# Optimization experiments

Measured on AMD Instinct MI355X. Metric: run time of the kernel, lower is better.

Reference implementation:

```python
import jax, jax.numpy as jnp
import numpy as np

N_NODES = 20000
N_EDGES = 160000
D = 1000          # out_channels of GatedGraphConv / Linear in-dim
NUM_LAYERS = 3


def setup_inputs() -> dict:
    key = jax.random.key(0)
    ks = jax.random.split(key, 10)
    x = jax.random.normal(ks[0], (N_NODES, D), dtype=jnp.float32)
    edge_index = jax.random.randint(ks[1], (2, N_EDGES), 0, N_NODES, dtype=jnp.int32)
    edge_weight = jax.random.uniform(ks[2], (N_EDGES,), dtype=jnp.float32)
    s = 1.0 / np.sqrt(D)
    weight = jax.random.uniform(ks[3], (NUM_LAYERS, D, D), minval=-s, maxval=s, dtype=jnp.float32)
    w_ih = jax.random.uniform(ks[4], (3 * D, D), minval=-s, maxval=s, dtype=jnp.float32)
    w_hh = jax.random.uniform(ks[5], (3 * D, D), minval=-s, maxval=s, dtype=jnp.float32)
    b_ih = jax.random.uniform(ks[6], (3 * D,), minval=-s, maxval=s, dtype=jnp.float32)
    b_hh = jax.random.uniform(ks[7], (3 * D,), minval=-s, maxval=s, dtype=jnp.float32)
    fc_w = jax.random.uniform(ks[8], (1, D), minval=-s, maxval=s, dtype=jnp.float32)
    fc_b = jax.random.uniform(ks[9], (1,), minval=-s, maxval=s, dtype=jnp.float32)
    return {
        "x": x, "edge_index": edge_index, "edge_weight": edge_weight,
        "weight": weight, "w_ih": w_ih, "w_hh": w_hh, "b_ih": b_ih, "b_hh": b_hh,
        "fc_w": fc_w, "fc_b": fc_b, "prob": 0,
    }


def _gru_cell(m, h, w_ih, w_hh, b_ih, b_hh):
    # torch.nn.GRUCell: gate order r, z, n
    gi = m @ w_ih.T + b_ih   # [N, 3D]
    gh = h @ w_hh.T + b_hh   # [N, 3D]
    i_r, i_z, i_n = jnp.split(gi, 3, axis=-1)
    h_r, h_z, h_n = jnp.split(gh, 3, axis=-1)
    r = jax.nn.sigmoid(i_r + h_r)
    z = jax.nn.sigmoid(i_z + h_z)
    n = jnp.tanh(i_n + r * h_n)
    return (1.0 - z) * n + z * h


def reference(x, edge_index, edge_weight, weight, w_ih, w_hh, b_ih, b_hh, fc_w, fc_b, prob):
    src = edge_index[0]
    dst = edge_index[1]
    h = x
    for layer in range(NUM_LAYERS):
        m = h @ weight[layer]                                  # [N, D]
        msg = m[src] * edge_weight[:, None]                    # [E, D]
        agg = jax.ops.segment_sum(msg, dst, num_segments=N_NODES)  # scatter-add
        h = _gru_cell(agg, h, w_ih, w_hh, b_ih, b_hh)
    h = jax.nn.relu(h)
    # F.dropout with p=prob=0 is identity (scale 1/(1-0)=1)
    return h @ fc_w.T + fc_b                                   # [N, 1]
```

## Files before the change

kernel.cpp:

```cpp
#include <hip/hip_runtime.h>

typedef unsigned short u16;
typedef unsigned int u32;
typedef unsigned long long u64;
typedef __attribute__((ext_vector_type(8))) short bf16x8;
typedef __attribute__((ext_vector_type(4))) float f32x4;

#define N_NODES 20000
#define N_EDGES 160000
#define DDIM    1000
#define KP      1024
#define SP      41200000
#define WCAT_L  6291456

__device__ __forceinline__ float b2f(u16 u) {
    union { u32 i; float f; } v; v.i = ((u32)u) << 16; return v.f;
}
__device__ __forceinline__ u16 f2b(float f) {
    union { float f; u32 i; } v; v.f = f;
    u32 r = v.i + 0x7FFFu + ((v.i >> 16) & 1u);
    return (u16)(r >> 16);
}
__device__ __forceinline__ u32 pack2(float a, float b) {
    return (u32)f2b(a) | ((u32)f2b(b) << 16);
}
__device__ __forceinline__ f32x4 mfma16(bf16x8 a, bf16x8 b, f32x4 c) {
    return __builtin_amdgcn_mfma_f32_16x16x32_bf16(a, b, c, 0, 0, 0);
}
__device__ __forceinline__ float fexp_(float x) {
    return __builtin_amdgcn_exp2f(x * 1.4426950408889634f);
}
__device__ __forceinline__ float fsigmoid_(float x) {
    return __builtin_amdgcn_rcpf(1.0f + fexp_(-x));
}
__device__ __forceinline__ float ftanh_(float x) {
    float ax = fabsf(x);
    float e = fexp_(-2.0f * ax);
    float t = (1.0f - e) * __builtin_amdgcn_rcpf(1.0f + e);
    return x >= 0.0f ? t : -t;
}

__device__ __forceinline__ void gl2lds16(const u16* g, u16* l) {
    __builtin_amdgcn_global_load_lds(
        (const __attribute__((address_space(1))) u32*)g,
        (__attribute__((address_space(3))) u32*)l, 16, 0, 0);
}
__device__ __forceinline__ u32 lds_addr(const u16* p) {
    return (u32)(uintptr_t)(const __attribute__((address_space(3))) u16*)p;
}

__global__ __launch_bounds__(256) void cvt_rows(const float* __restrict__ in,
                                                u16* __restrict__ out) {
    int r = blockIdx.x, c = threadIdx.x * 4;
    u32 o[2] = {0, 0};
    if (c < DDIM) {
        float4 v = *(const float4*)(in + (size_t)r * DDIM + c);
        o[0] = pack2(v.x, v.y); o[1] = pack2(v.z, v.w);
    }
    *(uint2*)(out + (size_t)r * KP + c) = *(const uint2*)o;
}

__global__ __launch_bounds__(256) void cvt_weights(const float* __restrict__ wih,
                                                   const float* __restrict__ W,
                                                   const float* __restrict__ whh,
                                                   u16* __restrict__ wihb,
                                                   u16* __restrict__ Wb3,
                                                   u16* __restrict__ wcat) {
    int b = blockIdx.x, c = threadIdx.x * 4;
    const float* src;
    u16* dst;
    if (b < 3000) {
        src = wih + (size_t)b * DDIM;
        dst = wihb + (size_t)b * KP;
    } else if (b < 6000) {
        int r = b - 3000;
        int l = r / 1000, row = r - l * 1000;
        src = W + (size_t)r * DDIM;
        dst = Wb3 + (size_t)l * 1048576 + (size_t)row * KP;
    } else {
        int r = b - 6000;
        int l = r / 3000, gr = r - l * 3000;
        int g = gr / 1000, n2 = gr - g * 1000;
        src = whh + (size_t)gr * DDIM;
        dst = wcat + (size_t)l * WCAT_L + ((size_t)g * 1024 + n2) * 2048 + 1024;
    }
    u32 o[2] = {0, 0};
    if (c < DDIM) {
        float4 v = *(const float4*)(src + c);
        o[0] = pack2(v.x, v.y); o[1] = pack2(v.z, v.w);
    }
    *(uint2*)(dst + c) = *(const uint2*)o;
}

__global__ __launch_bounds__(256) void count_edges(const int* __restrict__ ei,
                                                   int* __restrict__ cnt) {
    int e = blockIdx.x * 256 + threadIdx.x;
    if (e < N_EDGES) atomicAdd(&cnt[ei[N_EDGES + e]], 1);
}

__global__ __launch_bounds__(1024) void scan_offsets(const int* __restrict__ cnt,
                                                     int* __restrict__ ofs) {
    __shared__ int s[1024];
    const int CH = 20;
    int t = threadIdx.x;
    int base = t * CH;
    int loc[CH];
    int sum = 0;
    for (int j = 0; j < CH; j++) {
        int i = base + j;
        loc[j] = sum;
        sum += (i < N_NODES) ? cnt[i] : 0;
    }
    s[t] = sum;
    __syncthreads();
    for (int d = 1; d < 1024; d <<= 1) {
        int v = (t >= d) ? s[t - d] : 0;
        __syncthreads();
        s[t] += v;
        __syncthreads();
    }
    int excl = s[t] - sum;
    for (int j = 0; j < CH; j++) {
        int i = base + j;
        if (i < N_NODES) ofs[i] = excl + loc[j];
    }
    if (t == 0) ofs[N_NODES] = N_EDGES;
}

__global__ __launch_bounds__(256) void fill_buckets(const int* __restrict__ ei,
                                                    const int* __restrict__ ofs,
                                                    int* __restrict__ cur,
                                                    int* __restrict__ bkt) {
    int e = blockIdx.x * 256 + threadIdx.x;
    if (e >= N_EDGES) return;
    int d = ei[N_EDGES + e];
    int pos = atomicAdd(&cur[d], 1);
    bkt[ofs[d] + pos] = e;
}

__global__ __launch_bounds__(256) void node_agg(const int* __restrict__ ei,
                                                const float* __restrict__ ew,
                                                const int* __restrict__ ofs,
                                                const int* __restrict__ bkt,
                                                const u16* __restrict__ hsrc,
                                                u16* __restrict__ agg) {
    __shared__ int   s_src[2][32];
    __shared__ float s_w[2][32];
    __shared__ int   s_it[2];
    int tid = threadIdx.x;
    int half = tid >> 7, t = tid & 127;
    int node = blockIdx.x * 2 + half;
    int beg = ofs[node], end = ofs[node + 1];
    if (t == 0) s_it[half] = (end - beg + 31) >> 5;
    __syncthreads();
    int iters = max(s_it[0], s_it[1]);
    float acc[8] = {};
    for (int it = 0; it < iters; it++) {
        int cb = beg + it * 32;
        int n = min(32, end - cb);
        if (t < n) {
            int e = bkt[cb + t];
            s_src[half][t] = ei[e];
            s_w[half][t]   = ew[e];
        }
        __syncthreads();
        if (t < 125) {
            for (int j = 0; j < n; j++) {
                int src = s_src[half][j];
                float w = s_w[half][j];
                uint4 v = *(const uint4*)(hsrc + (size_t)src * KP + t * 8);
                const u16* p = (const u16*)&v;
#pragma unroll
                for (int k = 0; k < 8; k++) acc[k] += b2f(p[k]) * w;
            }
        }
        __syncthreads();
    }
    if (t < 125) {
        u32 o[4] = {pack2(acc[0], acc[1]), pack2(acc[2], acc[3]),
                    pack2(acc[4], acc[5]), pack2(acc[6], acc[7])};
        *(uint4*)(agg + (size_t)node * KP + t * 8) = *(const uint4*)o;
    } else if (t < 128) {
        uint4 z = {0, 0, 0, 0};
        *(uint4*)(agg + (size_t)node * KP + 1000 + (t - 125) * 8) = z;
    }
}

__global__ __launch_bounds__(256) void gemm_wc(const u16* __restrict__ A,
                                               const u16* __restrict__ Bt3,
                                               u16* __restrict__ wcat) {
    __shared__ u16 S[16384];
    int tid = threadIdx.x;
    int lane = tid & 63, wave = tid >> 6;
    int wr = wave >> 1, wc = wave & 1;
    int bid = blockIdx.x;
    int l = blockIdx.y;
    int m0 = (bid >> 3) * 128, n0 = (bid & 7) * 128;
    const u16* Bt = Bt3 + (size_t)l * 1048576;

    int aoff[4], boff[4];
#pragma unroll
    for (int i = 0; i < 4; i++) {
        int c = tid + 256 * i;
        int row = c >> 3, sl = c & 7;
        int kc = sl ^ (row & 7);
        aoff[i] = (m0 + row) * KP + kc * 8;
        boff[i] = (n0 + row) * KP + kc * 8;
    }
    f32x4 acc[4][4] = {};
    int fr = lane & 15, q = lane >> 4, sw = fr & 7;

    for (int k0 = 0; k0 < KP; k0 += 64) {
#pragma unroll
        for (int i = 0; i < 4; i++) {
            gl2lds16(A + aoff[i] + k0, &S[tid * 8 + 2048 * i]);
            gl2lds16(Bt + boff[i] + k0, &S[8192 + tid * 8 + 2048 * i]);
        }
        __syncthreads();
#pragma unroll
        for (int ks = 0; ks < 2; ks++) {
            int kx = ((ks * 4 + q) ^ sw) * 8;
            bf16x8 af[4], bf[4];
#pragma unroll
            for (int i = 0; i < 4; i++)
                af[i] = *(const bf16x8*)&S[(wr * 64 + i * 16 + fr) * 64 + kx];
#pragma unroll
            for (int j = 0; j < 4; j++)
                bf[j] = *(const bf16x8*)&S[8192 + (wc * 64 + j * 16 + fr) * 64 + kx];
#pragma unroll
            for (int i = 0; i < 4; i++)
#pragma unroll
                for (int j = 0; j < 4; j++)
                    acc[i][j] = mfma16(af[i], bf[j], acc[i][j]);
        }
        __syncthreads();
    }

    u16* wl = wcat + (size_t)l * WCAT_L;
    int cc = lane & 15, r4 = q * 4;
#pragma unroll
    for (int i = 0; i < 4; i++)
#pragma unroll
        for (int j = 0; j < 4; j++) {
            int gn = n0 + wc * 64 + j * 16 + cc;
            if (gn >= DDIM) continue;
#pragma unroll
            for (int r = 0; r < 4; r++) {
                int gm = m0 + wr * 64 + i * 16 + r4 + r;
                if (gm >= 3000) continue;
                int slab = (gm >= 2000) ? 2 : (gm >= 1000 ? 1 : 0);
                int row = gm - slab * 1000;
                wl[(size_t)slab * 2097152 + (size_t)row * 2048 + gn] =
                    f2b(acc[i][j][r]);
            }
        }
}

#define DSR(D, A)   asm volatile("ds_read_b128 %0, %1" : "=v"(D) : "v"(A))
#define DSR8(D, A)  asm volatile("ds_read_b128 %0, %1 offset:8192" : "=v"(D) : "v"(A))
#define DSR16(D, A) asm volatile("ds_read_b128 %0, %1 offset:16384" : "=v"(D) : "v"(A))
#define LGKM(N) do { asm volatile("s_waitcnt lgkmcnt(" #N ")" ::: "memory");  \
                     __builtin_amdgcn_sched_barrier(0); } while (0)
#define MF4(ACC, I, G) do {                                                   \
        ACC[I][0] = mfma16(af[I][0], wf[G][0][0], ACC[I][0]);                 \
        ACC[I][0] = mfma16(af[I][1], wf[G][0][1], ACC[I][0]);                 \
        ACC[I][1] = mfma16(af[I][0], wf[G][1][0], ACC[I][1]);                 \
        ACC[I][1] = mfma16(af[I][1], wf[G][1][1], ACC[I][1]);                 \
    } while (0)

__global__ __launch_bounds__(512, 2) void gru_fused(const u16* __restrict__ agg,
                                                    const u16* __restrict__ h,
                                                    const u16* __restrict__ wcat,
                                                    const float* __restrict__ bih,
                                                    const float* __restrict__ bhh,
                                                    u16* __restrict__ hout) {
    extern __shared__ u16 S[];
    int tid = threadIdx.x;
    int lane = tid & 63, wave = tid >> 6;
    int wr = wave >> 1, wc = wave & 1;

    int bid = blockIdx.x;
    int xcd = bid & 7;
    int s = bid >> 3;
    int panel = s >> 1, hi = s & 1;
    int m0 = panel * 256;
    int n0 = (xcd * 2 + hi) * 64;

    int aoff[4];
#pragma unroll
    for (int i = 0; i < 4; i++) {
        int c = tid + 512 * i;
        int row = c >> 3, sl = c & 7;
        int kc = sl ^ (row & 7);
        aoff[i] = (m0 + row) * KP + kc * 8;
    }
    int wrow = tid >> 3;
    int woff = (n0 + wrow) * 2048 + ((tid & 7) ^ (wrow & 7)) * 8;

    f32x4 aR[4][2] = {}, aZ[4][2] = {}, aN[4][2] = {}, aH[4][2] = {};
    int fr = lane & 15, q = lane >> 4, sw = fr & 7;
    int kx0 = (q ^ sw) * 8, kx1 = ((4 + q) ^ sw) * 8;

    u32 afa[4][2], wfa[2][2];
#pragma unroll
    for (int i = 0; i < 4; i++) {
        int ar = (wr * 64 + i * 16 + fr) * 64;
        afa[i][0] = lds_addr(&S[ar + kx0]);
        afa[i][1] = lds_addr(&S[ar + kx1]);
    }
#pragma unroll
    for (int j = 0; j < 2; j++) {
        int wcl = (wc * 32 + j * 16 + fr) * 64;
        wfa[j][0] = lds_addr(&S[32768 + wcl + kx0]);
        wfa[j][1] = lds_addr(&S[32768 + wcl + kx1]);
    }

#define STAGE(ts) do {                                                        \
        const u16* ap_ = ((ts) < 16) ? agg : h;                               \
        int kb_ = ((ts) < 16) ? (ts) * 64 : (ts) * 64 - 1024;                 \
        int ab_ = ((ts) & 1) * 16384, wb_ = 32768 + ((ts) & 1) * 16384;       \
        _Pragma("unroll")                                                     \
        for (int i_ = 0; i_ < 4; i_++)                                        \
            gl2lds16(ap_ + aoff[i_] + kb_, &S[ab_ + tid * 8 + 4096 * i_]);    \
        int kw_ = (ts) * 64;                                                  \
        _Pragma("unroll")                                                     \
        for (int g_ = 0; g_ < 3; g_++)                                        \
            gl2lds16(wcat + (size_t)g_ * 2097152 + woff + kw_,                \
                     &S[wb_ + g_ * 4096 + tid * 8]);                          \
    } while (0)

    STAGE(0);
    asm volatile("s_waitcnt vmcnt(0)" ::: "memory");
    __builtin_amdgcn_s_barrier();

#pragma unroll 1
    for (int t = 0; t < 32; t++) {
        if (t <= 30) STAGE(t + 1);
        __builtin_amdgcn_sched_barrier(0);
        bf16x8 af[4][2], wf[3][2][2];
        DSR(wf[0][0][0], wfa[0][0]); DSR(wf[0][0][1], wfa[0][1]);
        DSR(wf[0][1][0], wfa[1][0]); DSR(wf[0][1][1], wfa[1][1]);
#pragma unroll
        for (int i = 0; i < 4; i++) {
            DSR(af[i][0], afa[i][0]); DSR(af[i][1], afa[i][1]);
        }
        LGKM(6);
        __builtin_amdgcn_s_setprio(1);
        MF4(aR, 0, 0);
        __builtin_amdgcn_s_setprio(0);
        DSR8(wf[1][0][0], wfa[0][0]); DSR8(wf[1][0][1], wfa[0][1]);
        DSR8(wf[1][1][0], wfa[1][0]); DSR8(wf[1][1][1], wfa[1][1]);
        LGKM(8);
        __builtin_amdgcn_s_setprio(1);
        MF4(aR, 1, 0);
        __builtin_amdgcn_s_setprio(0);
        DSR16(wf[2][0][0], wfa[0][0]); DSR16(wf[2][0][1], wfa[0][1]);
        DSR16(wf[2][1][0], wfa[1][0]); DSR16(wf[2][1][1], wfa[1][1]);
        LGKM(8);
        __builtin_amdgcn_s_setprio(1);
        MF4(aR, 2, 0); MF4(aR, 3, 0);
        __builtin_amdgcn_s_setprio(0);
        LGKM(4);
        __builtin_amdgcn_s_setprio(1);
        MF4(aZ, 0, 1); MF4(aZ, 1, 1); MF4(aZ, 2, 1); MF4(aZ, 3, 1);
        __builtin_amdgcn_s_setprio(0);
        LGKM(0);
        __builtin_amdgcn_s_setprio(1);
        if (t < 16) { MF4(aN, 0, 2); MF4(aN, 1, 2); MF4(aN, 2, 2); MF4(aN, 3, 2); }
        else        { MF4(aH, 0, 2); MF4(aH, 1, 2); MF4(aH, 2, 2); MF4(aH, 3, 2); }
        __builtin_amdgcn_s_setprio(0);
        __builtin_amdgcn_sched_barrier(0);
        if (t <= 30) {
            asm volatile("s_waitcnt vmcnt(0)" ::: "memory");
            __builtin_amdgcn_s_barrier();
        }
#pragma unroll
        for (int i = 0; i < 4; i++) { afa[i][0] ^= 0x8000u; afa[i][1] ^= 0x8000u; }
#pragma unroll
        for (int j = 0; j < 2; j++) { wfa[j][0] ^= 0x8000u; wfa[j][1] ^= 0x8000u; }
    }
#undef STAGE

    int cc = lane & 15, r4 = q * 4;
#pragma unroll
    for (int j = 0; j < 2; j++) {
        int gn = n0 + wc * 32 + j * 16 + cc;
        if (gn >= DDIM) continue;
        float br  = bih[gn] + bhh[gn];
        float bz  = bih[1000 + gn] + bhh[1000 + gn];
        float bni = bih[2000 + gn];
        float bnh = bhh[2000 + gn];
#pragma unroll
        for (int i = 0; i < 4; i++)
#pragma unroll
            for (int r = 0; r < 4; r++) {
                int gm = m0 + wr * 64 + i * 16 + r4 + r;
                if (gm >= N_NODES) continue;
                float rg = fsigmoid_(aR[i][j][r] + br);
                float zg = fsigmoid_(aZ[i][j][r] + bz);
                float ng = ftanh_(aN[i][j][r] + bni + rg * (aH[i][j][r] + bnh));
                size_t idx = (size_t)gm * KP + gn;
                float hp = b2f(h[idx]);
                hout[idx] = f2b((1.0f - zg) * ng + zg * hp);
            }
    }
}
#undef DSR
#undef DSR8
#undef DSR16
#undef LGKM
#undef MF4

__global__ __launch_bounds__(256) void fc_out(const u16* __restrict__ h,
                                              const float* __restrict__ fw,
                                              const float* __restrict__ fb,
                                              float* __restrict__ out) {
    int row = blockIdx.x * 4 + (threadIdx.x >> 6);
    int lane = threadIdx.x & 63;
    if (row >= N_NODES) return;
    float s = 0.0f;
#pragma unroll
    for (int i = 0; i < 2; i++) {
        int c = lane + 64 * i;
        if (c < 125) {
            uint4 v = *(const uint4*)(h + (size_t)row * KP + c * 8);
            const u16* pv = (const u16*)&v;
            float4 w0 = *(const float4*)(fw + c * 8);
            float4 w1 = *(const float4*)(fw + c * 8 + 4);
            const float* wp = (const float*)&w0;
            float hv;
#pragma unroll
            for (int k = 0; k < 4; k++) {
                hv = b2f(pv[k]);
                s += (hv > 0.0f ? hv : 0.0f) * wp[k];
            }
            wp = (const float*)&w1;
#pragma unroll
            for (int k = 0; k < 4; k++) {
                hv = b2f(pv[4 + k]);
                s += (hv > 0.0f ? hv : 0.0f) * wp[k];
            }
        }
    }
    for (int off = 32; off > 0; off >>= 1) s += __shfl_down(s, off, 64);
    if (lane == 0) out[row] = s + fb[0];
}

extern "C" void kernel_launch(void* const* d_in, const int* in_sizes, int n_in,
                              void* d_out, int out_size, void* d_ws, size_t ws_size,
                              hipStream_t stream) {
    const float* x   = (const float*)d_in[0];
    const int*   ei  = (const int*)d_in[1];
    const float* ew  = (const float*)d_in[2];
    const float* W   = (const float*)d_in[3];
    const float* wih = (const float*)d_in[4];
    const float* whh = (const float*)d_in[5];
    const float* bih = (const float*)d_in[6];
    const float* bhh = (const float*)d_in[7];
    const float* fw  = (const float*)d_in[8];
    const float* fb  = (const float*)d_in[9];
    float* out = (float*)d_out;

    hipFuncSetAttribute((const void*)gru_fused,
                        hipFuncAttributeMaxDynamicSharedMemorySize, 122880);

    char* ws = (char*)d_ws;
    u16* xb   = (u16*)(ws);
    u16* bufA = (u16*)(ws + (size_t)SP);
    u16* bufB = (u16*)(ws + (size_t)2 * SP);
    u16* wcat = (u16*)(ws + 123600000);
    int* cnt  = (int*)(ws + 161400000);
    int* cur  = (int*)(ws + 161480000);
    int* ofs  = (int*)(ws + 161560000);
    int* bkt  = (int*)(ws + 161640192);

    u16* wihb = bufA;
    u16* Wb3  = bufA + 3145728;

    cvt_rows<<<N_NODES, 256, 0, stream>>>(x, xb);
    cvt_weights<<<15000, 256, 0, stream>>>(wih, W, whh, wihb, Wb3, wcat);
    gemm_wc<<<dim3(192, 3), 256, 0, stream>>>(wihb, Wb3, wcat);
    hipMemsetAsync(cnt, 0, 160000, stream);
    count_edges<<<625, 256, 0, stream>>>(ei, cnt);
    scan_offsets<<<1, 1024, 0, stream>>>(cnt, ofs);
    fill_buckets<<<625, 256, 0, stream>>>(ei, ofs, cur, bkt);

    node_agg<<<10000, 256, 0, stream>>>(ei, ew, ofs, bkt, xb, bufB);
    gru_fused<<<1264, 512, 122880, stream>>>(bufB, xb, wcat, bih, bhh, bufA);

    node_agg<<<10000, 256, 0, stream>>>(ei, ew, ofs, bkt, bufA, bufB);
    gru_fused<<<1264, 512, 122880, stream>>>(bufB, bufA, wcat + WCAT_L, bih, bhh, xb);

    node_agg<<<10000, 256, 0, stream>>>(ei, ew, ofs, bkt, xb, bufB);
    gru_fused<<<1264, 512, 122880, stream>>>(bufB, xb, wcat + 2 * WCAT_L, bih, bhh, bufA);

    fc_out<<<5000, 256, 0, stream>>>(bufA, fw, fb, out);
}
```

Before: 1.161 ms.

## Pre-swizzle GRU weights into fragment order and load them directly to registers

The concatenated GRU weight matrix is now written, both by the conversion kernel and by the W·w_ih GEMM epilogue, in a layout that matches the MFMA B-fragment order per wave. gru_fused then loads weight fragments straight from global memory into registers with dwordx4 loads instead of staging them through LDS. Only the activation tile stays double-buffered in LDS. This halves the LDS footprint (122880 to 65536 bytes) and removes the LDS weight reads and writes. In exchange, each wave issues its own global weight loads with no reuse across waves, and the first loads of each iteration are not prefetched, so more latency may be exposed.

```diff
diff --git a/kernel.cpp b/kernel.cpp
--- a/kernel.cpp
+++ b/kernel.cpp
@@ -48,6 +48,7 @@
 __device__ __forceinline__ u32 lds_addr(const u16* p) {
     return (u32)(uintptr_t)(const __attribute__((address_space(3))) u16*)p;
 }
+
 
 __global__ __launch_bounds__(256) void cvt_rows(const float* __restrict__ in,
                                                 u16* __restrict__ out) {
@@ -67,22 +68,36 @@
                                                    u16* __restrict__ Wb3,
                                                    u16* __restrict__ wcat) {
     int b = blockIdx.x, c = threadIdx.x * 4;
+    if (b >= 6000) {
+        int r = b - 6000;
+        int l = r / 3000, gr = r - l * 3000;
+        int g = gr / 1000, n2 = gr - g * 1000;
+        const float* src = whh + (size_t)gr * DDIM;
+        u32 o[2] = {0, 0};
+        if (c < DDIM) {
+            float4 v = *(const float4*)(src + c);
+            o[0] = pack2(v.x, v.y); o[1] = pack2(v.z, v.w);
+        }
+        int sl = n2 >> 6, ns = n2 & 63;
+        int wcg = ns >> 5, j = (ns >> 4) & 1, fr = ns & 15;
+        int t = 16 + (c >> 6), kk = c & 63;
+        int kx = kk >> 5, q = (kk >> 3) & 3, e = kk & 7;
+        size_t idx = (((((size_t)(l * 16 + sl) * 2 + wcg) * 32 + t) * 3 + g)
+                      * 2 + j) * 2 + kx;
+        *(uint2*)((char*)wcat + idx * 1024 + (q * 16 + fr) * 16 + e * 2) =
+            *(const uint2*)o;
+        return;
+    }
     const float* src;
     u16* dst;
     if (b < 3000) {
         src = wih + (size_t)b * DDIM;
         dst = wihb + (size_t)b * KP;
-    } else if (b < 6000) {
+    } else {
         int r = b - 3000;
         int l = r / 1000, row = r - l * 1000;
         src = W + (size_t)r * DDIM;
         dst = Wb3 + (size_t)l * 1048576 + (size_t)row * KP;
-    } else {
-        int r = b - 6000;
-        int l = r / 3000, gr = r - l * 3000;
-        int g = gr / 1000, n2 = gr - g * 1000;
-        src = whh + (size_t)gr * DDIM;
-        dst = wcat + (size_t)l * WCAT_L + ((size_t)g * 1024 + n2) * 2048 + 1024;
     }
     u32 o[2] = {0, 0};
     if (c < DDIM) {
@@ -236,7 +251,6 @@
         __syncthreads();
     }
 
-    u16* wl = wcat + (size_t)l * WCAT_L;
     int cc = lane & 15, r4 = q * 4;
 #pragma unroll
     for (int i = 0; i < 4; i++)
@@ -244,22 +258,30 @@
         for (int j = 0; j < 4; j++) {
             int gn = n0 + wc * 64 + j * 16 + cc;
             if (gn >= DDIM) continue;
+            int t = gn >> 6, kk = gn & 63;
+            int kxo = kk >> 5, qk = (kk >> 3) & 3, e = kk & 7;
 #pragma unroll
             for (int r = 0; r < 4; r++) {
                 int gm = m0 + wr * 64 + i * 16 + r4 + r;
                 if (gm >= 3000) continue;
-                int slab = (gm >= 2000) ? 2 : (gm >= 1000 ? 1 : 0);
-                int row = gm - slab * 1000;
-                wl[(size_t)slab * 2097152 + (size_t)row * 2048 + gn] =
+                int g = (gm >= 2000) ? 2 : (gm >= 1000 ? 1 : 0);
+                int n = gm - g * 1000;
+                int sl = n >> 6, ns = n & 63;
+                int wcg = ns >> 5, jj = (ns >> 4) & 1, fr2 = ns & 15;
+                size_t idx = (((((size_t)(l * 16 + sl) * 2 + wcg) * 32 + t)
+                               * 3 + g) * 2 + jj) * 2 + kxo;
+                ((u16*)wcat)[idx * 512 + (qk * 16 + fr2) * 8 + e] =
                     f2b(acc[i][j][r]);
             }
         }
 }
 
-#define DSR(D, A)   asm volatile("ds_read_b128 %0, %1" : "=v"(D) : "v"(A))
-#define DSR8(D, A)  asm volatile("ds_read_b128 %0, %1 offset:8192" : "=v"(D) : "v"(A))
-#define DSR16(D, A) asm volatile("ds_read_b128 %0, %1 offset:16384" : "=v"(D) : "v"(A))
+#define DSR(D, A)  asm volatile("ds_read_b128 %0, %1" : "=v"(D) : "v"(A))
+#define GLD(D, A, OFF) asm volatile("global_load_dwordx4 %0, %1, off offset:" #OFF \
+        : "=v"(D) : "v"(A) : "memory")
 #define LGKM(N) do { asm volatile("s_waitcnt lgkmcnt(" #N ")" ::: "memory");  \
+                     __builtin_amdgcn_sched_barrier(0); } while (0)
+#define VMC(N)  do { asm volatile("s_waitcnt vmcnt(" #N ")" ::: "memory");    \
                      __builtin_amdgcn_sched_barrier(0); } while (0)
 #define MF4(ACC, I, G) do {                                                   \
         ACC[I][0] = mfma16(af[I][0], wf[G][0][0], ACC[I][0]);                 \
@@ -284,7 +306,8 @@
     int s = bid >> 3;
     int panel = s >> 1, hi = s & 1;
     int m0 = panel * 256;
-    int n0 = (xcd * 2 + hi) * 64;
+    int slice = xcd * 2 + hi;
+    int n0 = slice * 64;
 
     int aoff[4];
 #pragma unroll
@@ -294,92 +317,76 @@
         int kc = sl ^ (row & 7);
         aoff[i] = (m0 + row) * KP + kc * 8;
     }
-    int wrow = tid >> 3;
-    int woff = (n0 + wrow) * 2048 + ((tid & 7) ^ (wrow & 7)) * 8;
 
     f32x4 aR[4][2] = {}, aZ[4][2] = {}, aN[4][2] = {}, aH[4][2] = {};
     int fr = lane & 15, q = lane >> 4, sw = fr & 7;
     int kx0 = (q ^ sw) * 8, kx1 = ((4 + q) ^ sw) * 8;
 
-    u32 afa[4][2], wfa[2][2];
+    u32 afa[4][2];
 #pragma unroll
     for (int i = 0; i < 4; i++) {
         int ar = (wr * 64 + i * 16 + fr) * 64;
         afa[i][0] = lds_addr(&S[ar + kx0]);
         afa[i][1] = lds_addr(&S[ar + kx1]);
     }
-#pragma unroll
-    for (int j = 0; j < 2; j++) {
-        int wcl = (wc * 32 + j * 16 + fr) * 64;
-        wfa[j][0] = lds_addr(&S[32768 + wcl + kx0]);
-        wfa[j][1] = lds_addr(&S[32768 + wcl + kx1]);
-    }
-
-#define STAGE(ts) do {                                                        \
+    u64 wga0 = (u64)wcat + (u64)(u32)((slice * 2 + wc) * 393216)
+             + (u32)(lane * 16);
+    u64 wga1 = wga0 + 4096;
+    u64 wga2 = wga0 + 8192;
+
+#define STAGE_A(ts) do {                                                      \
         const u16* ap_ = ((ts) < 16) ? agg : h;                               \
         int kb_ = ((ts) < 16) ? (ts) * 64 : (ts) * 64 - 1024;                 \
-        int ab_ = ((ts) & 1) * 16384, wb_ = 32768 + ((ts) & 1) * 16384;       \
+        int ab_ = ((ts) & 1) * 16384;                                         \
         _Pragma("unroll")                                                     \
         for (int i_ = 0; i_ < 4; i_++)                                        \
             gl2lds16(ap_ + aoff[i_] + kb_, &S[ab_ + tid * 8 + 4096 * i_]);    \
-        int kw_ = (ts) * 64;                                                  \
-        _Pragma("unroll")                                                     \
-        for (int g_ = 0; g_ < 3; g_++)                                        \
-            gl2lds16(wcat + (size_t)g_ * 2097152 + woff + kw_,                \
-                     &S[wb_ + g_ * 4096 + tid * 8]);                          \
     } while (0)
 
-    STAGE(0);
+    STAGE_A(0);
     asm volatile("s_waitcnt vmcnt(0)" ::: "memory");
     __builtin_amdgcn_s_barrier();
 
 #pragma unroll 1
     for (int t = 0; t < 32; t++) {
-        if (t <= 30) STAGE(t + 1);
+        bf16x8 af[4][2], wf[3][2][2];
+        GLD(wf[0][0][0], wga0, 0);    GLD(wf[0][0][1], wga0, 1024);
+        GLD(wf[0][1][0], wga0, 2048); GLD(wf[0][1][1], wga0, 3072);
+        GLD(wf[1][0][0], wga1, 0);    GLD(wf[1][0][1], wga1, 1024);
+        GLD(wf[1][1][0], wga1, 2048); GLD(wf[1][1][1], wga1, 3072);
+        GLD(wf[2][0][0], wga2, 0);    GLD(wf[2][0][1], wga2, 1024);
+        GLD(wf[2][1][0], wga2, 2048); GLD(wf[2][1][1], wga2, 3072);
+        STAGE_A(t + 1);
         __builtin_amdgcn_sched_barrier(0);
-        bf16x8 af[4][2], wf[3][2][2];
-        DSR(wf[0][0][0], wfa[0][0]); DSR(wf[0][0][1], wfa[0][1]);
-        DSR(wf[0][1][0], wfa[1][0]); DSR(wf[0][1][1], wfa[1][1]);
 #pragma unroll
         for (int i = 0; i < 4; i++) {
             DSR(af[i][0], afa[i][0]); DSR(af[i][1], afa[i][1]);
         }
-        LGKM(6);
+        LGKM(4);
+        VMC(12);
         __builtin_amdgcn_s_setprio(1);
-        MF4(aR, 0, 0);
+        MF4(aR, 0, 0); MF4(aR, 1, 0);
         __builtin_amdgcn_s_setprio(0);
-        DSR8(wf[1][0][0], wfa[0][0]); DSR8(wf[1][0][1], wfa[0][1]);
-        DSR8(wf[1][1][0], wfa[1][0]); DSR8(wf[1][1][1], wfa[1][1]);
-        LGKM(8);
-        __builtin_amdgcn_s_setprio(1);
-        MF4(aR, 1, 0);
-        __builtin_amdgcn_s_setprio(0);
-        DSR16(wf[2][0][0], wfa[0][0]); DSR16(wf[2][0][1], wfa[0][1]);
-        DSR16(wf[2][1][0], wfa[1][0]); DSR16(wf[2][1][1], wfa[1][1]);
-        LGKM(8);
+        LGKM(0);
         __builtin_amdgcn_s_setprio(1);
         MF4(aR, 2, 0); MF4(aR, 3, 0);
         __builtin_amdgcn_s_setprio(0);
-        LGKM(4);
+        VMC(8);
         __builtin_amdgcn_s_setprio(1);
         MF4(aZ, 0, 1); MF4(aZ, 1, 1); MF4(aZ, 2, 1); MF4(aZ, 3, 1);
         __builtin_amdgcn_s_setprio(0);
-        LGKM(0);
+        VMC(4);
         __builtin_amdgcn_s_setprio(1);
         if (t < 16) { MF4(aN, 0, 2); MF4(aN, 1, 2); MF4(aN, 2, 2); MF4(aN, 3, 2); }
         else        { MF4(aH, 0, 2); MF4(aH, 1, 2); MF4(aH, 2, 2); MF4(aH, 3, 2); }
         __builtin_amdgcn_s_setprio(0);
-        __builtin_amdgcn_sched_barrier(0);
-        if (t <= 30) {
-            asm volatile("s_waitcnt vmcnt(0)" ::: "memory");
-            __builtin_amdgcn_s_barrier();
-        }
+        VMC(0);
+        __builtin_amdgcn_s_barrier();
 #pragma unroll
         for (int i = 0; i < 4; i++) { afa[i][0] ^= 0x8000u; afa[i][1] ^= 0x8000u; }
-#pragma unroll
-        for (int j = 0; j < 2; j++) { wfa[j][0] ^= 0x8000u; wfa[j][1] ^= 0x8000u; }
-    }
-#undef STAGE
+        wga0 += 12288; wga1 += 12288; wga2 += 12288;
+    }
+#undef STAGE_A
 
     int cc = lane & 15, r4 = q * 4;
 #pragma unroll
@@ -406,9 +413,9 @@
     }
 }
 #undef DSR
-#undef DSR8
-#undef DSR16
+#undef GLD
 #undef LGKM
+#undef VMC
 #undef MF4
 
 __global__ __launch_bounds__(256) void fc_out(const u16* __restrict__ h,
@@ -462,7 +469,7 @@
     float* out = (float*)d_out;
 
     hipFuncSetAttribute((const void*)gru_fused,
-                        hipFuncAttributeMaxDynamicSharedMemorySize, 122880);
+                        hipFuncAttributeMaxDynamicSharedMemorySize, 65536);
 
     char* ws = (char*)d_ws;
     u16* xb   = (u16*)(ws);
@@ -486,13 +493,13 @@
     fill_buckets<<<625, 256, 0, stream>>>(ei, ofs, cur, bkt);
 
     node_agg<<<10000, 256, 0, stream>>>(ei, ew, ofs, bkt, xb, bufB);
-    gru_fused<<<1264, 512, 122880, stream>>>(bufB, xb, wcat, bih, bhh, bufA);
+    gru_fused<<<1264, 512, 65536, stream>>>(bufB, xb, wcat, bih, bhh, bufA);
 
     node_agg<<<10000, 256, 0, stream>>>(ei, ew, ofs, bkt, bufA, bufB);
-    gru_fused<<<1264, 512, 122880, stream>>>(bufB, bufA, wcat + WCAT_L, bih, bhh, xb);
+    gru_fused<<<1264, 512, 65536, stream>>>(bufB, bufA, wcat + WCAT_L, bih, bhh, xb);
 
     node_agg<<<10000, 256, 0, stream>>>(ei, ew, ofs, bkt, xb, bufB);
-    gru_fused<<<1264, 512, 122880, stream>>>(bufB, xb, wcat + 2 * WCAT_L, bih, bhh, bufA);
+    gru_fused<<<1264, 512, 65536, stream>>>(bufB, xb, wcat + 2 * WCAT_L, bih, bhh, bufA);
 
     fc_out<<<5000, 256, 0, stream>>>(bufA, fw, fb, out);
 }
```

Result: no change. 1.183 ms (+1.9%).
